# Performance work log

Hardware: AMD Instinct MI355X
Metric: run time of the kernel (lower is better)

## Reference

```python
import jax, jax.numpy as jnp
import numpy as np

B, C, H, W = 4, 64, 160, 160
OUT, KH, KW = 64, 3, 3
STRIDE, PAD = 1, 1
K2 = KH * KW


def conv2d(x, w, b=None, stride=STRIDE, pad=PAD):
    y = jax.lax.conv_general_dilated(
        x, w, window_strides=(stride, stride),
        padding=[(pad, pad), (pad, pad)],
        dimension_numbers=("NCHW", "OIHW", "NCHW"))
    if b is not None:
        y = y + b[None, :, None, None]
    return y


def bilinear_gather(x, py, px):
    # x: [B,C,H,W]; py,px: [B,K2,Ho,Wo] float sampling positions
    Bq, Cq, Hq, Wq = x.shape
    y0 = jnp.floor(py)
    x0 = jnp.floor(px)
    wy1 = py - y0  # frac
    wx1 = px - x0
    y0i = y0.astype(jnp.int32)
    x0i = x0.astype(jnp.int32)
    x_flat = x.reshape(Bq, Cq, Hq * Wq)

    def corner(yi, xi, wgt):
        valid = (yi >= 0) & (yi < Hq) & (xi >= 0) & (xi < Wq)
        idx = jnp.clip(yi, 0, Hq - 1) * Wq + jnp.clip(xi, 0, Wq - 1)  # [B,K2,Ho,Wo]
        g = jax.vmap(lambda xf, i: jnp.take(xf, i, axis=1))(x_flat, idx)  # [B,C,K2,Ho,Wo]
        return g * (wgt * valid)[:, None]

    out = corner(y0i, x0i, (1 - wy1) * (1 - wx1))
    out = out + corner(y0i, x0i + 1, (1 - wy1) * wx1)
    out = out + corner(y0i + 1, x0i, wy1 * (1 - wx1))
    out = out + corner(y0i + 1, x0i + 1, wy1 * wx1)
    return out  # [B,C,K2,Ho,Wo]


def deform_forward(x, offset_w, offset_b, mask_w, mask_b, dcn_w):
    offset = conv2d(x, offset_w, offset_b)                # [B, 2*K2, Ho, Wo]
    mask = jax.nn.sigmoid(conv2d(x, mask_w, mask_b))      # [B, K2, Ho, Wo]
    Bq, _, Ho, Wo = offset.shape
    off = offset.reshape(Bq, K2, 2, Ho, Wo)
    off_y, off_x = off[:, :, 0], off[:, :, 1]
    k = jnp.arange(K2)
    ky = (k // KW).astype(jnp.float32)
    kx = (k % KW).astype(jnp.float32)
    base_i = jnp.arange(Ho, dtype=jnp.float32) * STRIDE - PAD
    base_j = jnp.arange(Wo, dtype=jnp.float32) * STRIDE - PAD
    py = off_y + base_i[None, None, :, None] + ky[None, :, None, None]
    px = off_x + base_j[None, None, None, :] + kx[None, :, None, None]
    sampled = bilinear_gather(x, py, px)                  # [B,C,K2,Ho,Wo]
    w = dcn_w.reshape(OUT, C, K2)
    # out[b,o,i,j] = sum_{c,k} w[o,c,k] * mask[b,k,i,j] * sampled[b,c,k,i,j]
    return jnp.einsum("ock,bckij,bkij->boij", w, sampled, mask)


def setup_inputs() -> dict:
    key = jax.random.key(0)
    ks = jax.random.split(key, 6)
    x = jax.random.normal(ks[0], (B, C, H, W), dtype=jnp.float32)
    # small random weights so offsets stay modest (module inits them to 0;
    # random values exercise the full deformable math)
    offset_w = jax.random.normal(ks[1], (2 * K2, C, KH, KW), dtype=jnp.float32) * 0.01
    offset_b = jax.random.normal(ks[2], (2 * K2,), dtype=jnp.float32) * 0.1
    mask_w = jax.random.normal(ks[3], (K2, C, KH, KW), dtype=jnp.float32) * 0.01
    mask_b = jax.random.normal(ks[4], (K2,), dtype=jnp.float32) * 0.1
    dcn_w = jax.random.normal(ks[5], (OUT, C, KH, KW), dtype=jnp.float32) * (1.0 / np.sqrt(C * K2))
    return {"x": x, "offset_w": offset_w, "offset_b": offset_b,
            "mask_w": mask_w, "mask_b": mask_b, "dcn_w": dcn_w}


def reference(x, offset_w, offset_b, mask_w, mask_b, dcn_w):
    return deform_forward(x, offset_w, offset_b, mask_w, mask_b, dcn_w)
```

## Files before the change

### kernel.cpp

```cpp
#include <hip/hip_runtime.h>
#include <hip/hip_bf16.h>
#include <math.h>

#define Bq 4
#define Cq 64
#define Hq 160
#define Wq 160
#define HWq (Hq*Wq)
#define K2q 9
#define OUTq 64
#define KKq 576
#define KS  18
#define SROW 584

typedef __attribute__((ext_vector_type(8))) short short8;
typedef __attribute__((ext_vector_type(4))) float float4v;
typedef unsigned short ushort_t;

__device__ __forceinline__ float bf2f(unsigned short u) {
    unsigned int v = ((unsigned int)u) << 16;
    return __builtin_bit_cast(float, v);
}
__device__ __forceinline__ unsigned short f2bf(float f) {
    unsigned int u = __builtin_bit_cast(unsigned int, f);
    unsigned int r = u + 0x7fffu + ((u >> 16) & 1u);
    return (unsigned short)(r >> 16);
}
__device__ __forceinline__ float bflo(unsigned int u) {
    return __builtin_bit_cast(float, u << 16);
}
__device__ __forceinline__ float bfhi(unsigned int u) {
    return __builtin_bit_cast(float, u & 0xffff0000u);
}

__global__ void __launch_bounds__(256) k_transpose_x(const float* __restrict__ x,
                                                     ushort_t* __restrict__ xt) {
    __shared__ float tile[64][65];
    int b = blockIdx.y, hw0 = blockIdx.x * 64;
    int lane = threadIdx.x & 63, grp = threadIdx.x >> 6;
#pragma unroll
    for (int i = 0; i < 16; ++i) {
        int c = grp*16 + i;
        tile[c][lane] = x[(b*Cq + c)*HWq + hw0 + lane];
    }
    __syncthreads();
#pragma unroll
    for (int i = 0; i < 16; ++i) {
        int hw = grp*16 + i;
        xt[((size_t)b*HWq + hw0 + hw)*64 + lane] = f2bf(tile[lane][hw]);
    }
}

__global__ void k_relayout(const float* __restrict__ dcn_w,
                           const float* __restrict__ off_w,
                           const float* __restrict__ msk_w,
                           ushort_t* __restrict__ wtf,
                           ushort_t* __restrict__ cwf2) {
    int id = blockIdx.x*256 + threadIdx.x;
    if (id < 4*KS*512) {
        int j = id & 7, lane = (id>>3) & 63, ks = (id>>9) % KS, g = id/(512*KS);
        int kk = ks*32 + (lane>>4)*8 + j;
        int c  = kk & 63, kt = kk >> 6;
        int m  = g*16 + (lane&15);
        wtf[id] = f2bf(dcn_w[m*KKq + c*9 + kt]);
    }
    int id2 = id - 4*KS*512;
    if (id2 >= 0 && id2 < 9*2*2*512) {
        int j = id2 & 7, lane = (id2>>3) & 63;
        int ks2 = (id2>>9) & 1, g = (id2>>10) & 1, k = id2 >> 11;
        int co = g*16 + (lane&15);
        int c  = ks2*32 + (lane>>4)*8 + j;
        float w = 0.f;
        if (co < 18)      w = off_w[co*KKq + c*9 + k];
        else if (co < 27) w = msk_w[(co-18)*KKq + c*9 + k];
        cwf2[id2] = f2bf(w);
    }
}

#define HSTRIDE 72
__global__ void __launch_bounds__(256, 8) k_offmask(const ushort_t* __restrict__ xt,
                                                    const ushort_t* __restrict__ cwf2,
                                                    const float* __restrict__ off_b,
                                                    const float* __restrict__ msk_b,
                                                    float* __restrict__ om) {
    __shared__ __align__(16) ushort_t halo[3*34*HSTRIDE];
    __shared__ float s_o[32*28];
    int blk = blockIdx.x;
    int jt = blk % 5, i = (blk/5) % Hq, b = blk/(5*Hq);
    int j0 = jt*32;
    int tid = threadIdx.x, lane = tid & 63, grp = tid >> 6;

    const ushort_t* xtb = xt + (size_t)b*HWq*64;
    for (int t = tid; t < 816; t += 256) {
        int seg = t >> 3, sub = t & 7;
        int ky = seg / 34, px = seg % 34;
        int y = i + ky - 1, xx = j0 + px - 1;
        uint4 v = {0u,0u,0u,0u};
        if (y >= 0 && y < Hq && xx >= 0 && xx < Wq)
            v = *(const uint4*)(xtb + ((size_t)y*Wq + xx)*64 + sub*8);
        *(uint4*)(halo + (ky*34 + px)*HSTRIDE + sub*8) = v;
    }
    __syncthreads();

    int gM = grp & 1, gN = grp >> 1;
    int n = lane & 15, quad = lane >> 4;
    float4v acc = {0.f,0.f,0.f,0.f};
#pragma unroll
    for (int k = 0; k < 9; ++k) {
        int ky = k/3, kx = k - (k/3)*3;
        const ushort_t* bbase = halo + (ky*34 + gN*16 + n + kx)*HSTRIDE + quad*8;
#pragma unroll
        for (int ks2 = 0; ks2 < 2; ++ks2) {
            short8 a  = *(const short8*)(cwf2 + (size_t)(((k*2+gM)*2+ks2)*512 + lane*8));
            short8 bf = *(const short8*)(bbase + ks2*32);
            acc = __builtin_amdgcn_mfma_f32_16x16x32_bf16(a, bf, acc, 0, 0, 0);
        }
    }
    int p = gN*16 + n;
#pragma unroll
    for (int r = 0; r < 4; ++r) {
        int co = gM*16 + quad*4 + r;
        if (co < 27) {
            float v = acc[r];
            if (co < 18) v += off_b[co];
            else { v += msk_b[co-18]; v = 1.f/(1.f + __expf(-v)); }
            s_o[p*28 + co] = v;
        }
    }
    __syncthreads();
    float* omrow = om + (size_t)((b*Hq + i)*Wq + j0)*27;
    for (int t = tid; t < 864; t += 256) {
        int p2 = t / 27, co2 = t - p2*27;
        omrow[t] = s_o[p2*28 + co2];
    }
}

__global__ void __launch_bounds__(256, 6) k_deform(const ushort_t* __restrict__ xt,
                                                   const float* __restrict__ om,
                                                   const ushort_t* __restrict__ wtf,
                                                   float* __restrict__ out) {
    __shared__ __align__(16) ushort_t s_s[16*SROW];
    __shared__ __align__(16) unsigned int s_pk[144*12];
    int blk = blockIdx.x;
    int jt = blk % 10, i = (blk/10) % Hq, b = blk/(10*Hq);
    int j0 = jt*16;
    int tid = threadIdx.x, lane = tid & 63, grp = tid >> 6;

    if (tid < 144) {
        int p = tid & 15, k = tid >> 4;
        const float* op = om + (size_t)((b*Hq + i)*Wq + j0 + p)*27;
        float oy = op[2*k], ox = op[2*k+1], m = op[18+k];
        float py = oy + (float)(i - 1 + k/3);
        float px = ox + (float)(j0 + p - 1 + (k - (k/3)*3));
        float fy = floorf(py), fx = floorf(px);
        int y0 = (int)fy, x0 = (int)fx;
        float wy1 = py - fy, wx1 = px - fx;
        float wy0 = 1.f - wy1, wx0 = 1.f - wx1;
        bool vy0 = (y0 >= 0) & (y0 < Hq),   vy1 = (y0+1 >= 0) & (y0+1 < Hq);
        bool vx0 = (x0 >= 0) & (x0 < Wq),   vx1 = (x0+1 >= 0) & (x0+1 < Wq);
        int yc0 = min(max(y0,   0), Hq-1), yc1 = min(max(y0+1, 0), Hq-1);
        int xc0 = min(max(x0,   0), Wq-1), xc1 = min(max(x0+1, 0), Wq-1);
        unsigned int* pk = s_pk + tid*12;
        pk[0] = (unsigned int)((yc0*Wq + xc0)*128);
        pk[1] = (unsigned int)((yc0*Wq + xc1)*128);
        pk[2] = (unsigned int)((yc1*Wq + xc0)*128);
        pk[3] = (unsigned int)((yc1*Wq + xc1)*128);
        pk[4] = __builtin_bit_cast(unsigned int, (vy0 && vx0) ? wy0*wx0*m : 0.f);
        pk[5] = __builtin_bit_cast(unsigned int, (vy0 && vx1) ? wy0*wx1*m : 0.f);
        pk[6] = __builtin_bit_cast(unsigned int, (vy1 && vx0) ? wy1*wx0*m : 0.f);
        pk[7] = __builtin_bit_cast(unsigned int, (vy1 && vx1) ? wy1*wx1*m : 0.f);
        pk[8] = (unsigned int)(p*(SROW*2) + k*128);
    }
    __syncthreads();

    int lane4 = (lane & 31) * 4;
    int halfi = lane >> 5;
    const char* xtb = (const char*)(xt + (size_t)b*HWq*64);
    char* s_sb = (char*)s_s;
#pragma unroll 2
    for (int iter = 0; iter < 18; ++iter) {
        int t2h = iter*8 + grp*2 + halfi;
        const uint4* pkp = (const uint4*)(s_pk + t2h*12);
        uint4 A  = pkp[0];
        uint4 Wt = pkp[1];
        unsigned int dst = s_pk[t2h*12 + 8];
        unsigned int u00 = *(const unsigned int*)(xtb + A.x + lane4);
        unsigned int u01 = *(const unsigned int*)(xtb + A.y + lane4);
        unsigned int u10 = *(const unsigned int*)(xtb + A.z + lane4);
        unsigned int u11 = *(const unsigned int*)(xtb + A.w + lane4);
        float w00 = __builtin_bit_cast(float, Wt.x);
        float w01 = __builtin_bit_cast(float, Wt.y);
        float w10 = __builtin_bit_cast(float, Wt.z);
        float w11 = __builtin_bit_cast(float, Wt.w);
        float sl = w00*bflo(u00) + w01*bflo(u01) + w10*bflo(u10) + w11*bflo(u11);
        float sh = w00*bfhi(u00) + w01*bfhi(u01) + w10*bfhi(u10) + w11*bfhi(u11);
        __hip_bfloat162 h2 = __float22bfloat162_rn(make_float2(sl, sh));
        *(__hip_bfloat162*)(s_sb + dst + lane4) = h2;
    }
    __syncthreads();

    int n = lane & 15, quad = lane >> 4;
    float4v acc = {0.f,0.f,0.f,0.f};
    const ushort_t* arow = wtf + ((size_t)(grp*KS)*64 + lane)*8;
    const ushort_t* brow = s_s + n*SROW + quad*8;
#pragma unroll
    for (int ks = 0; ks < KS; ++ks) {
        short8 a  = *(const short8*)(arow + ks*512);
        short8 bf = *(const short8*)(brow + ks*32);
        acc = __builtin_amdgcn_mfma_f32_16x16x32_bf16(a, bf, acc, 0, 0, 0);
    }

#pragma unroll
    for (int r = 0; r < 4; ++r) {
        int o = grp*16 + quad*4 + r;
        out[(((size_t)b*OUTq + o)*Hq + i)*Wq + j0 + n] = acc[r];
    }
}

extern "C" void kernel_launch(void* const* d_in, const int* in_sizes, int n_in,
                              void* d_out, int out_size, void* d_ws, size_t ws_size,
                              hipStream_t stream) {
    const float* x     = (const float*)d_in[0];
    const float* off_w = (const float*)d_in[1];
    const float* off_b = (const float*)d_in[2];
    const float* msk_w = (const float*)d_in[3];
    const float* msk_b = (const float*)d_in[4];
    const float* dcn_w = (const float*)d_in[5];
    float* out = (float*)d_out;

    char* ws = (char*)d_ws;
    ushort_t* xt   = (ushort_t*)ws;
    float*    om   = (float*)(ws + (size_t)Bq*HWq*64*2);
    ushort_t* wtf  = (ushort_t*)((char*)om + (size_t)Bq*HWq*27*4);
    ushort_t* cwf2 = wtf + 4*KS*512;

    hipLaunchKernelGGL(k_transpose_x, dim3(HWq/64, Bq), dim3(256), 0, stream, x, xt);
    hipLaunchKernelGGL(k_relayout, dim3((4*KS*512 + 9*2*2*512)/256), dim3(256),
                       0, stream, dcn_w, off_w, msk_w, wtf, cwf2);
    hipLaunchKernelGGL(k_offmask, dim3(Bq*Hq*5), dim3(256), 0, stream,
                       xt, cwf2, off_b, msk_b, om);
    hipLaunchKernelGGL(k_deform, dim3(Bq*Hq*10), dim3(256), 0, stream,
                       xt, om, wtf, out);
}
```

Before: 144.5 us.

## Fuse offset/mask conv into deform kernel and merge prep kernels

Merges the transpose and weight relayout kernels into one prep kernel, and fuses the offset/mask convolution into the deformable sampling kernel, so the offset/mask values stay in shared memory instead of going through a global buffer. The conv is split across wave pairs over K halves and summed on readback. This removes two launches and the om round trip, at the cost of recomputing the halo per 16-pixel tile with a smaller MFMA N-tile. The transpose store is also widened to packed 32-bit writes.

```diff
diff --git a/kernel.cpp b/kernel.cpp
--- a/kernel.cpp
+++ b/kernel.cpp
@@ -12,15 +12,12 @@
 #define KKq 576
 #define KS  18
 #define SROW 584
+#define HSTRIDE 72
 
 typedef __attribute__((ext_vector_type(8))) short short8;
 typedef __attribute__((ext_vector_type(4))) float float4v;
 typedef unsigned short ushort_t;
 
-__device__ __forceinline__ float bf2f(unsigned short u) {
-    unsigned int v = ((unsigned int)u) << 16;
-    return __builtin_bit_cast(float, v);
-}
 __device__ __forceinline__ unsigned short f2bf(float f) {
     unsigned int u = __builtin_bit_cast(unsigned int, f);
     unsigned int r = u + 0x7fffu + ((u >> 16) & 1u);
@@ -33,123 +30,109 @@
     return __builtin_bit_cast(float, u & 0xffff0000u);
 }
 
-__global__ void __launch_bounds__(256) k_transpose_x(const float* __restrict__ x,
-                                                     ushort_t* __restrict__ xt) {
+__global__ void __launch_bounds__(256) k_prep(const float* __restrict__ x,
+                                              const float* __restrict__ dcn_w,
+                                              const float* __restrict__ off_w,
+                                              const float* __restrict__ msk_w,
+                                              ushort_t* __restrict__ xt,
+                                              ushort_t* __restrict__ wtf,
+                                              ushort_t* __restrict__ cwf2) {
     __shared__ float tile[64][65];
     int b = blockIdx.y, hw0 = blockIdx.x * 64;
-    int lane = threadIdx.x & 63, grp = threadIdx.x >> 6;
+    int tid = threadIdx.x;
+    int lane = tid & 63, grp = tid >> 6;
 #pragma unroll
     for (int i = 0; i < 16; ++i) {
         int c = grp*16 + i;
         tile[c][lane] = x[(b*Cq + c)*HWq + hw0 + lane];
     }
     __syncthreads();
-#pragma unroll
-    for (int i = 0; i < 16; ++i) {
-        int hw = grp*16 + i;
-        xt[((size_t)b*HWq + hw0 + hw)*64 + lane] = f2bf(tile[lane][hw]);
-    }
-}
-
-__global__ void k_relayout(const float* __restrict__ dcn_w,
-                           const float* __restrict__ off_w,
-                           const float* __restrict__ msk_w,
-                           ushort_t* __restrict__ wtf,
-                           ushort_t* __restrict__ cwf2) {
-    int id = blockIdx.x*256 + threadIdx.x;
-    if (id < 4*KS*512) {
-        int j = id & 7, lane = (id>>3) & 63, ks = (id>>9) % KS, g = id/(512*KS);
-        int kk = ks*32 + (lane>>4)*8 + j;
-        int c  = kk & 63, kt = kk >> 6;
-        int m  = g*16 + (lane&15);
-        wtf[id] = f2bf(dcn_w[m*KKq + c*9 + kt]);
-    }
-    int id2 = id - 4*KS*512;
-    if (id2 >= 0 && id2 < 9*2*2*512) {
-        int j = id2 & 7, lane = (id2>>3) & 63;
-        int ks2 = (id2>>9) & 1, g = (id2>>10) & 1, k = id2 >> 11;
-        int co = g*16 + (lane&15);
-        int c  = ks2*32 + (lane>>4)*8 + j;
-        float w = 0.f;
-        if (co < 18)      w = off_w[co*KKq + c*9 + k];
-        else if (co < 27) w = msk_w[(co-18)*KKq + c*9 + k];
-        cwf2[id2] = f2bf(w);
-    }
-}
-
-#define HSTRIDE 72
-__global__ void __launch_bounds__(256, 8) k_offmask(const ushort_t* __restrict__ xt,
-                                                    const ushort_t* __restrict__ cwf2,
-                                                    const float* __restrict__ off_b,
-                                                    const float* __restrict__ msk_b,
-                                                    float* __restrict__ om) {
-    __shared__ __align__(16) ushort_t halo[3*34*HSTRIDE];
-    __shared__ float s_o[32*28];
+    int cp = tid & 31, hwg = tid >> 5;
+#pragma unroll
+    for (int it = 0; it < 8; ++it) {
+        int hw = it*8 + hwg;
+        unsigned int v = (unsigned int)f2bf(tile[2*cp][hw])
+                       | ((unsigned int)f2bf(tile[2*cp+1][hw]) << 16);
+        *(unsigned int*)(xt + ((size_t)b*HWq + hw0 + hw)*64 + 2*cp) = v;
+    }
+    if (blockIdx.y == 0 && blockIdx.x < 216) {
+        int id = blockIdx.x*256 + tid;
+        if (id < 4*KS*512) {
+            int j = id & 7, ln = (id>>3) & 63, ks = (id>>9) % KS, g = id/(512*KS);
+            int kk = ks*32 + (ln>>4)*8 + j;
+            int c  = kk & 63, kt = kk >> 6;
+            int m  = g*16 + (ln&15);
+            wtf[id] = f2bf(dcn_w[m*KKq + c*9 + kt]);
+        }
+        int id2 = id - 4*KS*512;
+        if (id2 >= 0 && id2 < 9*2*2*512) {
+            int j = id2 & 7, ln = (id2>>3) & 63;
+            int ks2 = (id2>>9) & 1, g = (id2>>10) & 1, k = id2 >> 11;
+            int co = g*16 + (ln&15);
+            int c  = ks2*32 + (ln>>4)*8 + j;
+            float w = 0.f;
+            if (co < 18)      w = off_w[co*KKq + c*9 + k];
+            else if (co < 27) w = msk_w[(co-18)*KKq + c*9 + k];
+            cwf2[id2] = f2bf(w);
+        }
+    }
+}
+
+__global__ void __launch_bounds__(256, 6) k_fused(const ushort_t* __restrict__ xt,
+                                                  const ushort_t* __restrict__ cwf2,
+                                                  const float* __restrict__ off_b,
+                                                  const float* __restrict__ msk_b,
+                                                  const ushort_t* __restrict__ wtf,
+                                                  float* __restrict__ out) {
+    __shared__ __align__(16) char s_mem[16*SROW*2];
+    __shared__ __align__(16) unsigned int s_pk[144*12];
+    ushort_t* halo   = (ushort_t*)s_mem;
+    float*    s_part = (float*)(s_mem + 7776);
+    ushort_t* s_s    = (ushort_t*)s_mem;
+
     int blk = blockIdx.x;
-    int jt = blk % 5, i = (blk/5) % Hq, b = blk/(5*Hq);
-    int j0 = jt*32;
+    int jt = blk % 10, i = (blk/10) % Hq, b = blk/(10*Hq);
+    int j0 = jt*16;
     int tid = threadIdx.x, lane = tid & 63, grp = tid >> 6;
+    int n = lane & 15, quad = lane >> 4;
 
     const ushort_t* xtb = xt + (size_t)b*HWq*64;
-    for (int t = tid; t < 816; t += 256) {
+    for (int t = tid; t < 432; t += 256) {
         int seg = t >> 3, sub = t & 7;
-        int ky = seg / 34, px = seg % 34;
+        int ky = seg / 18, px = seg % 18;
         int y = i + ky - 1, xx = j0 + px - 1;
         uint4 v = {0u,0u,0u,0u};
         if (y >= 0 && y < Hq && xx >= 0 && xx < Wq)
             v = *(const uint4*)(xtb + ((size_t)y*Wq + xx)*64 + sub*8);
-        *(uint4*)(halo + (ky*34 + px)*HSTRIDE + sub*8) = v;
-    }
-    __syncthreads();
-
-    int gM = grp & 1, gN = grp >> 1;
-    int n = lane & 15, quad = lane >> 4;
-    float4v acc = {0.f,0.f,0.f,0.f};
-#pragma unroll
-    for (int k = 0; k < 9; ++k) {
-        int ky = k/3, kx = k - (k/3)*3;
-        const ushort_t* bbase = halo + (ky*34 + gN*16 + n + kx)*HSTRIDE + quad*8;
-#pragma unroll
-        for (int ks2 = 0; ks2 < 2; ++ks2) {
+        *(uint4*)(halo + (ky*18 + px)*HSTRIDE + sub*8) = v;
+    }
+    __syncthreads();
+
+    {
+        int gM = grp & 1, kh = grp >> 1;
+        float4v cacc = {0.f,0.f,0.f,0.f};
+#pragma unroll
+        for (int s = 0; s < 9; ++s) {
+            int st = kh*9 + s;
+            int k = st >> 1, ks2 = st & 1;
+            int ky = k/3, kx = k - (k/3)*3;
             short8 a  = *(const short8*)(cwf2 + (size_t)(((k*2+gM)*2+ks2)*512 + lane*8));
-            short8 bf = *(const short8*)(bbase + ks2*32);
-            acc = __builtin_amdgcn_mfma_f32_16x16x32_bf16(a, bf, acc, 0, 0, 0);
+            short8 bf = *(const short8*)(halo + (ky*18 + n + kx)*HSTRIDE + quad*8 + ks2*32);
+            cacc = __builtin_amdgcn_mfma_f32_16x16x32_bf16(a, bf, cacc, 0, 0, 0);
         }
-    }
-    int p = gN*16 + n;
-#pragma unroll
-    for (int r = 0; r < 4; ++r) {
-        int co = gM*16 + quad*4 + r;
-        if (co < 27) {
-            float v = acc[r];
-            if (co < 18) v += off_b[co];
-            else { v += msk_b[co-18]; v = 1.f/(1.f + __expf(-v)); }
-            s_o[p*28 + co] = v;
-        }
-    }
-    __syncthreads();
-    float* omrow = om + (size_t)((b*Hq + i)*Wq + j0)*27;
-    for (int t = tid; t < 864; t += 256) {
-        int p2 = t / 27, co2 = t - p2*27;
-        omrow[t] = s_o[p2*28 + co2];
-    }
-}
-
-__global__ void __launch_bounds__(256, 6) k_deform(const ushort_t* __restrict__ xt,
-                                                   const float* __restrict__ om,
-                                                   const ushort_t* __restrict__ wtf,
-                                                   float* __restrict__ out) {
-    __shared__ __align__(16) ushort_t s_s[16*SROW];
-    __shared__ __align__(16) unsigned int s_pk[144*12];
-    int blk = blockIdx.x;
-    int jt = blk % 10, i = (blk/10) % Hq, b = blk/(10*Hq);
-    int j0 = jt*16;
-    int tid = threadIdx.x, lane = tid & 63, grp = tid >> 6;
+        *(float4v*)(s_part + grp*256 + lane*4) = cacc;
+    }
+    __syncthreads();
 
     if (tid < 144) {
         int p = tid & 15, k = tid >> 4;
-        const float* op = om + (size_t)((b*Hq + i)*Wq + j0 + p)*27;
-        float oy = op[2*k], ox = op[2*k+1], m = op[18+k];
+        #define RD(co) (s_part[(((co)>>4)*256)       + ((((co)&15)>>2)*16 + p)*4 + ((co)&3)] + \
+                        s_part[(2 + ((co)>>4))*256   + ((((co)&15)>>2)*16 + p)*4 + ((co)&3)])
+        float oy = RD(2*k)   + off_b[2*k];
+        float ox = RD(2*k+1) + off_b[2*k+1];
+        float mv = RD(18+k)  + msk_b[k];
+        #undef RD
+        float m = 1.f/(1.f + __expf(-mv));
         float py = oy + (float)(i - 1 + k/3);
         float px = ox + (float)(j0 + p - 1 + (k - (k/3)*3));
         float fy = floorf(py), fx = floorf(px);
@@ -175,7 +158,7 @@
 
     int lane4 = (lane & 31) * 4;
     int halfi = lane >> 5;
-    const char* xtb = (const char*)(xt + (size_t)b*HWq*64);
+    const char* xtbB = (const char*)xtb;
     char* s_sb = (char*)s_s;
 #pragma unroll 2
     for (int iter = 0; iter < 18; ++iter) {
@@ -184,10 +167,10 @@
         uint4 A  = pkp[0];
         uint4 Wt = pkp[1];
         unsigned int dst = s_pk[t2h*12 + 8];
-        unsigned int u00 = *(const unsigned int*)(xtb + A.x + lane4);
-        unsigned int u01 = *(const unsigned int*)(xtb + A.y + lane4);
-        unsigned int u10 = *(const unsigned int*)(xtb + A.z + lane4);
-        unsigned int u11 = *(const unsigned int*)(xtb + A.w + lane4);
+        unsigned int u00 = *(const unsigned int*)(xtbB + A.x + lane4);
+        unsigned int u01 = *(const unsigned int*)(xtbB + A.y + lane4);
+        unsigned int u10 = *(const unsigned int*)(xtbB + A.z + lane4);
+        unsigned int u11 = *(const unsigned int*)(xtbB + A.w + lane4);
         float w00 = __builtin_bit_cast(float, Wt.x);
         float w01 = __builtin_bit_cast(float, Wt.y);
         float w10 = __builtin_bit_cast(float, Wt.z);
@@ -199,7 +182,6 @@
     }
     __syncthreads();
 
-    int n = lane & 15, quad = lane >> 4;
     float4v acc = {0.f,0.f,0.f,0.f};
     const ushort_t* arow = wtf + ((size_t)(grp*KS)*64 + lane)*8;
     const ushort_t* brow = s_s + n*SROW + quad*8;
@@ -230,15 +212,11 @@
 
     char* ws = (char*)d_ws;
     ushort_t* xt   = (ushort_t*)ws;
-    float*    om   = (float*)(ws + (size_t)Bq*HWq*64*2);
-    ushort_t* wtf  = (ushort_t*)((char*)om + (size_t)Bq*HWq*27*4);
+    ushort_t* wtf  = xt + (size_t)Bq*HWq*64;
     ushort_t* cwf2 = wtf + 4*KS*512;
 
-    hipLaunchKernelGGL(k_transpose_x, dim3(HWq/64, Bq), dim3(256), 0, stream, x, xt);
-    hipLaunchKernelGGL(k_relayout, dim3((4*KS*512 + 9*2*2*512)/256), dim3(256),
-                       0, stream, dcn_w, off_w, msk_w, wtf, cwf2);
-    hipLaunchKernelGGL(k_offmask, dim3(Bq*Hq*5), dim3(256), 0, stream,
-                       xt, cwf2, off_b, msk_b, om);
-    hipLaunchKernelGGL(k_deform, dim3(Bq*Hq*10), dim3(256), 0, stream,
-                       xt, om, wtf, out);
-}
+    hipLaunchKernelGGL(k_prep, dim3(HWq/64, Bq), dim3(256), 0, stream,
+                       x, dcn_w, off_w, msk_w, xt, wtf, cwf2);
+    hipLaunchKernelGGL(k_fused, dim3(Bq*Hq*10), dim3(256), 0, stream,
+                       xt, cwf2, off_b, msk_b, wtf, out);
+}
```

Result: faster. 134.5 us (-6.9%).
